# Kernel optimization log

Hardware: AMD Instinct MI355X
Metric: run time of the kernel (lower is better)

## Reference

```python
import jax, jax.numpy as jnp
import numpy as np

B, C, T, H, W = 16, 16, 32, 64, 64
SCALES = [1, 2, 4, 8]
HEADS, HD = 4, 8  # head_dim = T // heads
LN_EPS = 1e-5


def setup_inputs() -> dict:
    key = jax.random.key(0)
    ks = jax.random.split(key, 12)
    return {
        "x": jax.random.normal(ks[0], (B, C, T, H, W), dtype=jnp.float32),
        # Conv1d(1 -> T, k=3, padding=1)
        "conv_w": jax.random.normal(ks[1], (T, 1, 3), dtype=jnp.float32) * 0.1,
        "conv_b": jax.random.normal(ks[2], (T,), dtype=jnp.float32) * 0.1,
        "scale_weights": jnp.ones((len(SCALES),), dtype=jnp.float32),
        "decay_alpha": jnp.float32(0.1),
        "decay_beta": jnp.float32(0.1),
        "temporal_importance": jnp.ones((T,), dtype=jnp.float32),
        "attn_key": jax.random.normal(ks[3], (HEADS, HD), dtype=jnp.float32) * 0.1,
        "attn_value": jax.random.normal(ks[4], (HEADS, HD), dtype=jnp.float32) * 0.1,
        "pos_encoding": jax.random.normal(ks[5], (T,), dtype=jnp.float32) * 0.02,
        "proj_w": jax.random.normal(ks[6], (T, T), dtype=jnp.float32) * 0.05,
        "proj_b": jnp.zeros((T,), dtype=jnp.float32),
        "temporal_dynamics": jax.random.normal(ks[7], (T,), dtype=jnp.float32) * 0.1,
        "ln_gamma": jnp.ones((T,), dtype=jnp.float32),
        "ln_beta": jnp.zeros((T,), dtype=jnp.float32),
    }


def _conv3_mean(xs, wbar, bbar):
    # conv1d(1->T,k=3,pad=1) followed by mean over the T output channels ==
    # conv with channel-averaged kernel wbar[3] and bias bbar. xs: [B,C,Ts]
    xp = jnp.pad(xs, ((0, 0), (0, 0), (1, 1)))
    return wbar[0] * xp[..., :-2] + wbar[1] * xp[..., 1:-1] + wbar[2] * xp[..., 2:] + bbar


def _temporal_lin_interp(y, t_out):
    # F.interpolate trilinear, align_corners=False, on the temporal axis only
    ts = y.shape[-1]
    if ts == t_out:
        return y
    pos = (jnp.arange(t_out, dtype=jnp.float32) + 0.5) * (ts / t_out) - 0.5
    pos = jnp.clip(pos, 0.0, ts - 1.0)
    i0 = jnp.floor(pos).astype(jnp.int32)
    i1 = jnp.minimum(i0 + 1, ts - 1)
    w = pos - i0.astype(jnp.float32)
    return y[..., i0] * (1.0 - w) + y[..., i1] * w


def reference(x, conv_w, conv_b, scale_weights, decay_alpha, decay_beta,
              temporal_importance, attn_key, attn_value, pos_encoding,
              proj_w, proj_b, temporal_dynamics, ln_gamma, ln_beta):
    b, c, t, h, w = x.shape
    xt = x.mean(axis=(3, 4))  # [B,C,T] spatial mean (adaptive_avg_pool3d keeps H,W)
    wbar = conv_w.mean(axis=0)[0]  # [3]
    bbar = conv_b.mean()
    # Multi-scale: each scale output is constant over H,W (comes from [B,C,Ts,1,1]),
    # so carry everything as [B,C,T] and broadcast at the end -- same math.
    xm = jnp.zeros_like(xt)
    for i, s in enumerate(SCALES):
        xs = xt if s == 1 else xt.reshape(b, c, t // s, s).mean(axis=-1)
        y = _conv3_mean(xs, wbar, bbar)
        xm = xm + scale_weights[i] * _temporal_lin_interp(y, t)
    # Adaptive temporal decay
    ts_idx = jnp.arange(t, dtype=jnp.float32)
    ad = jnp.exp(-decay_alpha * ts_idx) * jax.nn.sigmoid(decay_beta * ts_idx) \
         * jax.nn.sigmoid(temporal_importance)
    xm = xm * ad
    # Multi-head temporal attention (softmax over a length-1 axis == 1,
    # so head_output is the value vector broadcast; computed literally here)
    xf = xm.reshape(b * c, t) + pos_encoding
    xh = xf.reshape(b * c, HEADS, HD)
    scores = jnp.einsum('nhd,hd->nh', xh, attn_key)[..., None]  # [BC,H,1]
    probs = jax.nn.softmax(scores, axis=-1)                      # all ones
    head_out = probs * attn_value[None, :, :]                    # [BC,H,HD]
    attn = head_out.reshape(b * c, t) @ proj_w.T + proj_b
    xm = xm * attn.reshape(b, c, t)
    # LayerNorm(sigmoid(temporal_dynamics)) temporal weighting, then sum over T
    tw = jax.nn.sigmoid(temporal_dynamics)
    twn = (tw - tw.mean()) / jnp.sqrt(tw.var() + LN_EPS) * ln_gamma + ln_beta
    pooled_t = (xm * twn).sum(axis=-1)  # [B,C]
    return jnp.broadcast_to(pooled_t[:, :, None, None], (b, c, h, w))
```

## Files before the change

### kernel.cpp

```cpp
#include <hip/hip_runtime.h>
#include <math.h>

#define B_ 16
#define C_ 16
#define T_ 32
#define H_ 64
#define W_ 64
#define HW_ (H_ * W_)
#define BC_ (B_ * C_)
#define PER_BC_ ((size_t)T_ * HW_)

__device__ __forceinline__ double dsigmoid(double v) { return 1.0 / (1.0 + exp(-v)); }

__global__ void etad_precompute(
    const float* __restrict__ conv_w,
    const float* __restrict__ conv_b,
    const float* __restrict__ scale_w,
    const float* __restrict__ alpha_p,
    const float* __restrict__ beta_p,
    const float* __restrict__ ti,
    const float* __restrict__ av,
    const float* __restrict__ proj_w,
    const float* __restrict__ proj_b,
    const float* __restrict__ td,
    const float* __restrict__ ln_g,
    const float* __restrict__ ln_b,
    float* __restrict__ u_out)
{
    const int lane = threadIdx.x;
    const int t = lane & 31;

    double w0 = 0, w1 = 0, w2 = 0, bb = 0;
    for (int ch = 0; ch < T_; ++ch) {
        w0 += (double)conv_w[ch * 3 + 0];
        w1 += (double)conv_w[ch * 3 + 1];
        w2 += (double)conv_w[ch * 3 + 2];
        bb += (double)conv_b[ch];
    }
    w0 /= T_; w1 /= T_; w2 /= T_; bb /= T_;

    double tw = dsigmoid((double)td[t]);
    double s1 = tw;
    for (int m = 1; m < 32; m <<= 1) s1 += __shfl_xor(s1, m, 64);
    double mean = s1 / 32.0;
    double dv = tw - mean;
    double s2 = dv * dv;
    for (int m = 1; m < 32; m <<= 1) s2 += __shfl_xor(s2, m, 64);
    double var = s2 / 32.0;
    double twn = (tw - mean) / sqrt(var + 1e-5) * (double)ln_g[t] + (double)ln_b[t];

    double attn = (double)proj_b[t];
    for (int k = 0; k < 32; ++k) attn += (double)av[k] * (double)proj_w[t * 32 + k];

    double a = (double)alpha_p[0], be = (double)beta_p[0];
    double ad = exp(-a * (double)t) * dsigmoid(be * (double)t) * dsigmoid((double)ti[t]);

    double wt = ad * attn * twn;

    __shared__ double wsh[32];
    if (lane < 32) wsh[t] = wt;
    __syncthreads();

    double sumw = 0;
    for (int k = 0; k < 32; ++k) sumw += wsh[k];
    double sws = (double)scale_w[0] + (double)scale_w[1] + (double)scale_w[2] + (double)scale_w[3];
    double c0 = sumw * bb * sws;

    double v = 0;
    for (int i = 0; i < 4; ++i) {
        const int s = 1 << i;
        const int Ts = 32 >> i;
        const int jc = t / s;
        const double swi = (double)scale_w[i];
        const double inv_s = 1.0 / (double)s;
        for (int t2 = 0; t2 < 32; ++t2) {
            double pos = ((double)t2 + 0.5) * ((double)Ts / 32.0) - 0.5;
            if (pos < 0.0) pos = 0.0;
            const double mx = (double)(Ts - 1);
            if (pos > mx) pos = mx;
            int i0 = (int)floor(pos);
            int i1 = i0 + 1; if (i1 > Ts - 1) i1 = Ts - 1;
            double f = pos - (double)i0;
            int d0 = i0 - jc, d1 = i1 - jc;
            double y0 = (d0 == 1) ? w0 : ((d0 == 0) ? w1 : ((d0 == -1) ? w2 : 0.0));
            double y1 = (d1 == 1) ? w0 : ((d1 == 0) ? w1 : ((d1 == -1) ? w2 : 0.0));
            double coef = ((1.0 - f) * y0 + f * y1) * inv_s;
            v += swi * wsh[t2] * coef;
        }
    }

    if (lane < 32) u_out[t] = (float)(v / (double)HW_);
    if (lane == 0) u_out[32] = (float)c0;
}

__global__ __launch_bounds__(1024) void etad_main(
    const float* __restrict__ x, const float* __restrict__ u, float* __restrict__ out)
{
    const int bc = blockIdx.x;
    const int tid = threadIdx.x;

    __shared__ float su[33];
    if (tid < 33) su[tid] = u[tid];
    __syncthreads();

    const float4* xb = (const float4*)(x + (size_t)bc * PER_BC_);
    float acc = 0.f;
#pragma unroll
    for (int t = 0; t < T_; ++t) {
        float4 v = xb[t * (HW_ / 4) + tid];
        acc = fmaf(su[t], (v.x + v.y) + (v.z + v.w), acc);
    }

    for (int off = 32; off; off >>= 1) acc += __shfl_down(acc, off, 64);

    __shared__ float wsum[16];
    __shared__ float pooled_s;
    const int wid = tid >> 6;
    if ((tid & 63) == 0) wsum[wid] = acc;
    __syncthreads();
    if (tid == 0) {
        float s = 0.f;
#pragma unroll
        for (int i = 0; i < 16; ++i) s += wsum[i];
        pooled_s = s + su[32];
    }
    __syncthreads();

    const float p = pooled_s;
    float4 o = make_float4(p, p, p, p);
    ((float4*)(out + (size_t)bc * HW_))[tid] = o;
}

extern "C" void kernel_launch(void* const* d_in, const int* in_sizes, int n_in,
                              void* d_out, int out_size, void* d_ws, size_t ws_size,
                              hipStream_t stream) {
    const float* x      = (const float*)d_in[0];
    const float* conv_w = (const float*)d_in[1];
    const float* conv_b = (const float*)d_in[2];
    const float* sw     = (const float*)d_in[3];
    const float* alpha  = (const float*)d_in[4];
    const float* beta   = (const float*)d_in[5];
    const float* ti     = (const float*)d_in[6];
    const float* av     = (const float*)d_in[8];
    const float* pw     = (const float*)d_in[10];
    const float* pb     = (const float*)d_in[11];
    const float* td     = (const float*)d_in[12];
    const float* lg     = (const float*)d_in[13];
    const float* lb     = (const float*)d_in[14];

    float* out = (float*)d_out;
    float* u   = (float*)d_ws;

    etad_precompute<<<1, 64, 0, stream>>>(conv_w, conv_b, sw, alpha, beta, ti,
                                          av, pw, pb, td, lg, lb, u);
    etad_main<<<BC_, 1024, 0, stream>>>(x, u, out);
}
```

Measured before the change: 232.8 us.

## Fuse weight precompute into main reduction kernel and reduce per-timestep sums first

Merges the single-block precompute kernel into the streaming reduction kernel, so each block computes the 33 temporal weights redundantly in wave 0 instead of reading them from a workspace written by a prior launch. The main loop now has each wave sum two timesteps' planes unweighted, then applies the weights once per timestep at the end. This removes one launch and the dependency between the two kernels. In exchange, every block repeats the double-precision weight computation, which may delay wave 0's loads.

```diff
diff --git a/kernel.cpp b/kernel.cpp
--- a/kernel.cpp
+++ b/kernel.cpp
@@ -12,7 +12,8 @@
 
 __device__ __forceinline__ double dsigmoid(double v) { return 1.0 / (1.0 + exp(-v)); }
 
-__global__ void etad_precompute(
+__global__ __launch_bounds__(1024) void etad_fused(
+    const float* __restrict__ x,
     const float* __restrict__ conv_w,
     const float* __restrict__ conv_b,
     const float* __restrict__ scale_w,
@@ -25,110 +26,108 @@
     const float* __restrict__ td,
     const float* __restrict__ ln_g,
     const float* __restrict__ ln_b,
-    float* __restrict__ u_out)
+    float* __restrict__ out)
 {
-    const int lane = threadIdx.x;
-    const int t = lane & 31;
+    const int tid  = threadIdx.x;
+    const int lane = tid & 63;
+    const int wid  = tid >> 6;
+    const int bc   = blockIdx.x;
 
-    double w0 = 0, w1 = 0, w2 = 0, bb = 0;
-    for (int ch = 0; ch < T_; ++ch) {
-        w0 += (double)conv_w[ch * 3 + 0];
-        w1 += (double)conv_w[ch * 3 + 1];
-        w2 += (double)conv_w[ch * 3 + 2];
-        bb += (double)conv_b[ch];
+    __shared__ float su[33];
+    __shared__ float S[32];
+    __shared__ float pooled_s;
+
+    if (wid == 0) {
+        const int t = lane & 31;
+
+        double w0 = 0, w1 = 0, w2 = 0, bb = 0;
+        for (int ch = 0; ch < T_; ++ch) {
+            w0 += (double)conv_w[ch * 3 + 0];
+            w1 += (double)conv_w[ch * 3 + 1];
+            w2 += (double)conv_w[ch * 3 + 2];
+            bb += (double)conv_b[ch];
+        }
+        w0 /= T_; w1 /= T_; w2 /= T_; bb /= T_;
+
+        double tw = dsigmoid((double)td[t]);
+        double s1 = tw;
+        for (int m = 1; m < 32; m <<= 1) s1 += __shfl_xor(s1, m, 64);
+        double mean = s1 / 32.0;
+        double dv = tw - mean;
+        double s2 = dv * dv;
+        for (int m = 1; m < 32; m <<= 1) s2 += __shfl_xor(s2, m, 64);
+        double var = s2 / 32.0;
+        double twn = (tw - mean) / sqrt(var + 1e-5) * (double)ln_g[t] + (double)ln_b[t];
+
+        double attn = (double)proj_b[t];
+        for (int k = 0; k < 32; ++k) attn += (double)av[k] * (double)proj_w[t * 32 + k];
+
+        double a = (double)alpha_p[0], be = (double)beta_p[0];
+        double ad = exp(-a * (double)t) * dsigmoid(be * (double)t) * dsigmoid((double)ti[t]);
+
+        double wt = ad * attn * twn;
+
+        double sumw = wt;
+        for (int m = 1; m < 32; m <<= 1) sumw += __shfl_xor(sumw, m, 64);
+        double sws = (double)scale_w[0] + (double)scale_w[1] + (double)scale_w[2] + (double)scale_w[3];
+        double c0 = sumw * bb * sws;
+
+        double v = 0;
+        for (int i = 0; i < 4; ++i) {
+            const int s = 1 << i;
+            const int Ts = 32 >> i;
+            const int jc = t >> i;
+            const double swi = (double)scale_w[i];
+            const double inv_s = 1.0 / (double)s;
+            for (int t2 = 0; t2 < 32; ++t2) {
+                double pos = ((double)t2 + 0.5) * ((double)Ts / 32.0) - 0.5;
+                if (pos < 0.0) pos = 0.0;
+                const double mx = (double)(Ts - 1);
+                if (pos > mx) pos = mx;
+                int i0 = (int)floor(pos);
+                int i1 = i0 + 1; if (i1 > Ts - 1) i1 = Ts - 1;
+                double f = pos - (double)i0;
+                int d0 = i0 - jc, d1 = i1 - jc;
+                double y0 = (d0 == 1) ? w0 : ((d0 == 0) ? w1 : ((d0 == -1) ? w2 : 0.0));
+                double y1 = (d1 == 1) ? w0 : ((d1 == 0) ? w1 : ((d1 == -1) ? w2 : 0.0));
+                double coef = ((1.0 - f) * y0 + f * y1) * inv_s;
+                double wt2 = __shfl(wt, t2, 32);
+                v += swi * wt2 * coef;
+            }
+        }
+
+        if (lane < 32) su[t] = (float)(v / (double)HW_);
+        if (lane == 0) su[32] = (float)c0;
     }
-    w0 /= T_; w1 /= T_; w2 /= T_; bb /= T_;
 
-    double tw = dsigmoid((double)td[t]);
-    double s1 = tw;
-    for (int m = 1; m < 32; m <<= 1) s1 += __shfl_xor(s1, m, 64);
-    double mean = s1 / 32.0;
-    double dv = tw - mean;
-    double s2 = dv * dv;
-    for (int m = 1; m < 32; m <<= 1) s2 += __shfl_xor(s2, m, 64);
-    double var = s2 / 32.0;
-    double twn = (tw - mean) / sqrt(var + 1e-5) * (double)ln_g[t] + (double)ln_b[t];
-
-    double attn = (double)proj_b[t];
-    for (int k = 0; k < 32; ++k) attn += (double)av[k] * (double)proj_w[t * 32 + k];
-
-    double a = (double)alpha_p[0], be = (double)beta_p[0];
-    double ad = exp(-a * (double)t) * dsigmoid(be * (double)t) * dsigmoid((double)ti[t]);
-
-    double wt = ad * attn * twn;
-
-    __shared__ double wsh[32];
-    if (lane < 32) wsh[t] = wt;
+    const float4* xb = (const float4*)(x + (size_t)bc * PER_BC_);
+    const float4* p0 = xb + (size_t)(2 * wid) * (HW_ / 4) + lane;
+    const float4* p1 = p0 + (HW_ / 4);
+    float acc0 = 0.f, acc1 = 0.f;
+#pragma unroll
+    for (int i = 0; i < 16; ++i) {
+        float4 a4 = p0[i * 64];
+        float4 b4 = p1[i * 64];
+        acc0 += (a4.x + a4.y) + (a4.z + a4.w);
+        acc1 += (b4.x + b4.y) + (b4.z + b4.w);
+    }
+    for (int off = 32; off; off >>= 1) {
+        acc0 += __shfl_down(acc0, off, 64);
+        acc1 += __shfl_down(acc1, off, 64);
+    }
+    if (lane == 0) { S[2 * wid] = acc0; S[2 * wid + 1] = acc1; }
     __syncthreads();
 
-    double sumw = 0;
-    for (int k = 0; k < 32; ++k) sumw += wsh[k];
-    double sws = (double)scale_w[0] + (double)scale_w[1] + (double)scale_w[2] + (double)scale_w[3];
-    double c0 = sumw * bb * sws;
-
-    double v = 0;
-    for (int i = 0; i < 4; ++i) {
-        const int s = 1 << i;
-        const int Ts = 32 >> i;
-        const int jc = t / s;
-        const double swi = (double)scale_w[i];
-        const double inv_s = 1.0 / (double)s;
-        for (int t2 = 0; t2 < 32; ++t2) {
-            double pos = ((double)t2 + 0.5) * ((double)Ts / 32.0) - 0.5;
-            if (pos < 0.0) pos = 0.0;
-            const double mx = (double)(Ts - 1);
-            if (pos > mx) pos = mx;
-            int i0 = (int)floor(pos);
-            int i1 = i0 + 1; if (i1 > Ts - 1) i1 = Ts - 1;
-            double f = pos - (double)i0;
-            int d0 = i0 - jc, d1 = i1 - jc;
-            double y0 = (d0 == 1) ? w0 : ((d0 == 0) ? w1 : ((d0 == -1) ? w2 : 0.0));
-            double y1 = (d1 == 1) ? w0 : ((d1 == 0) ? w1 : ((d1 == -1) ? w2 : 0.0));
-            double coef = ((1.0 - f) * y0 + f * y1) * inv_s;
-            v += swi * wsh[t2] * coef;
-        }
-    }
-
-    if (lane < 32) u_out[t] = (float)(v / (double)HW_);
-    if (lane == 0) u_out[32] = (float)c0;
-}
-
-__global__ __launch_bounds__(1024) void etad_main(
-    const float* __restrict__ x, const float* __restrict__ u, float* __restrict__ out)
-{
-    const int bc = blockIdx.x;
-    const int tid = threadIdx.x;
-
-    __shared__ float su[33];
-    if (tid < 33) su[tid] = u[tid];
-    __syncthreads();
-
-    const float4* xb = (const float4*)(x + (size_t)bc * PER_BC_);
-    float acc = 0.f;
+    if (tid == 0) {
+        float pooled = su[32];
 #pragma unroll
-    for (int t = 0; t < T_; ++t) {
-        float4 v = xb[t * (HW_ / 4) + tid];
-        acc = fmaf(su[t], (v.x + v.y) + (v.z + v.w), acc);
-    }
-
-    for (int off = 32; off; off >>= 1) acc += __shfl_down(acc, off, 64);
-
-    __shared__ float wsum[16];
-    __shared__ float pooled_s;
-    const int wid = tid >> 6;
-    if ((tid & 63) == 0) wsum[wid] = acc;
-    __syncthreads();
-    if (tid == 0) {
-        float s = 0.f;
-#pragma unroll
-        for (int i = 0; i < 16; ++i) s += wsum[i];
-        pooled_s = s + su[32];
+        for (int t = 0; t < T_; ++t) pooled = fmaf(su[t], S[t], pooled);
+        pooled_s = pooled;
     }
     __syncthreads();
 
     const float p = pooled_s;
-    float4 o = make_float4(p, p, p, p);
-    ((float4*)(out + (size_t)bc * HW_))[tid] = o;
+    ((float4*)(out + (size_t)bc * HW_))[tid] = make_float4(p, p, p, p);
 }
 
 extern "C" void kernel_launch(void* const* d_in, const int* in_sizes, int n_in,
@@ -149,9 +148,7 @@
     const float* lb     = (const float*)d_in[14];
 
     float* out = (float*)d_out;
-    float* u   = (float*)d_ws;
 
-    etad_precompute<<<1, 64, 0, stream>>>(conv_w, conv_b, sw, alpha, beta, ti,
-                                          av, pw, pb, td, lg, lb, u);
-    etad_main<<<BC_, 1024, 0, stream>>>(x, u, out);
+    etad_fused<<<BC_, 1024, 0, stream>>>(x, conv_w, conv_b, sw, alpha, beta, ti,
+                                         av, pw, pb, td, lg, lb, out);
 }
```

Result: faster. 213.7 us (-8.2%).
